# Kernel optimization log

Hardware: AMD Instinct MI355X
Metric: run time of the kernel (lower is better)

Reference implementation:

```python
import jax, jax.numpy as jnp
import numpy as np

EPS = 1e-8  # torch CosineSimilarity default eps

B, T, D, K = 16, 1024, 2048, 64


def setup_inputs() -> dict:
    key = jax.random.key(0)
    k1, k2, k3 = jax.random.split(key, 3)
    inputs = jax.random.normal(k1, (B, T, D), dtype=jnp.float32)
    class_avgs = jax.random.normal(k2, (K, D), dtype=jnp.float32)
    labels = jax.random.randint(k3, (B, T), 0, K, dtype=jnp.int64)
    return {"inputs": inputs, "class_avgs": class_avgs, "labels": labels}


def _simrel_forward(inputs, class_avgs, labels):
    # inputs: [B, T, D]; class_avgs: [K, D]; labels: [B, T] int
    # Faithful training-mode forward: sequential running-mean prototype
    # update per token (row-major over batch then sequence), cosine sims
    # computed against the prototype state *before* each token's update.
    b, t, d = inputs.shape
    k = class_avgs.shape[0]
    vecs = inputs.reshape(b * t, d)
    labs = labels.reshape(b * t)
    class_ids = jnp.arange(k)

    def step(carry, xs):
        avgs, counts = carry          # [K, D], [K]
        vec, label = xs               # [D], scalar int
        nv = jnp.maximum(jnp.sqrt(jnp.sum(vec * vec)), EPS)
        na = jnp.maximum(jnp.sqrt(jnp.sum(avgs * avgs, axis=1)), EPS)  # [K]
        cos = (avgs @ vec) / (na * nv)                                 # [K]
        is_inf = jnp.any(jnp.isinf(avgs), axis=1)                      # [K]
        self_sim = jnp.sum(vec * vec) / (nv * nv)  # cosine(vec, vec)
        is_label = class_ids == label
        sims = jnp.where(is_inf, jnp.where(is_label, self_sim, -1.0), cos)
        # running-mean update of the labeled class prototype
        c = counts[label]
        old = avgs[label]
        new_row = jnp.where(is_inf[label], vec, (old * c + vec) / (c + 1.0))
        avgs = avgs.at[label].set(new_row)
        counts = counts.at[label].add(1.0)
        return (avgs, counts), sims

    counts0 = jnp.zeros((k,), dtype=inputs.dtype)
    (_, _), sims = jax.lax.scan(step, (class_avgs, counts0), (vecs, labs))
    return sims.reshape(b, t, k)


def reference(inputs, class_avgs, labels):
    return _simrel_forward(inputs, class_avgs, labels)
```

## Files before the change

### kernel.cpp

```cpp
#include <hip/hip_runtime.h>
#include <hip/hip_bf16.h>

#define N_TOK 16384
#define DIM 2048
#define KCLS 64
#define JRANGES 32
#define RANGE 512
#define KC 64
#define EPS 1e-8f

typedef short bf16x8 __attribute__((ext_vector_type(8)));
typedef unsigned short u16x8 __attribute__((ext_vector_type(8)));
typedef float f32x4 __attribute__((ext_vector_type(4)));

__device__ __forceinline__ unsigned short f2bf(float f) {
    unsigned u = __float_as_uint(f);
    u += 0x7fffu + ((u >> 16) & 1u);
    return (unsigned short)(u >> 16);
}
__device__ __forceinline__ float bf2f(unsigned short s) {
    return __uint_as_float(((unsigned)s) << 16);
}

__device__ __forceinline__ float dpp_sum64(float x) {
    x += __int_as_float(__builtin_amdgcn_update_dpp(0, __float_as_int(x), 0x111, 0xf, 0xf, true));
    x += __int_as_float(__builtin_amdgcn_update_dpp(0, __float_as_int(x), 0x112, 0xf, 0xf, true));
    x += __int_as_float(__builtin_amdgcn_update_dpp(0, __float_as_int(x), 0x114, 0xf, 0xf, true));
    x += __int_as_float(__builtin_amdgcn_update_dpp(0, __float_as_int(x), 0x118, 0xf, 0xf, true));
    x += __int_as_float(__builtin_amdgcn_update_dpp(0, __float_as_int(x), 0x142, 0xf, 0xf, true));
    x += __int_as_float(__builtin_amdgcn_update_dpp(0, __float_as_int(x), 0x143, 0xf, 0xf, true));
    return x;
}

__global__ __launch_bounds__(256) void prep_kernel(
    const float* __restrict__ x, unsigned short* __restrict__ xb,
    float* __restrict__ vnorm2, const int* __restrict__ raw,
    int* __restrict__ lab, float* __restrict__ n2snap) {
    int bid = blockIdx.x, tid = threadIdx.x;
    if (bid < 64) {
        __shared__ int not64;
        if (tid == 0) not64 = 0;
        __syncthreads();
        int n0 = bid * 256 + tid;
        int lo = raw[2 * n0], hi = raw[2 * n0 + 1];
        if (hi != 0 || lo < 0 || lo >= KCLS) atomicOr(&not64, 1);
        __syncthreads();
        lab[n0] = not64 ? raw[n0] : raw[2 * n0];
    } else if (bid < 72) {
        n2snap[(bid - 64) * 256 + tid] = 0.f;
    }
    int w4 = tid >> 6, lane = tid & 63;
    int n = bid * 4 + w4;
    const float* v = x + (size_t)n * DIM;
    unsigned short* o = xb + (size_t)n * DIM;
    float p = 0.f;
#pragma unroll
    for (int it = 0; it < 8; it++) {
        float4 a = *(const float4*)(v + it * 256 + lane * 4);
        p = fmaf(a.x, a.x, p); p = fmaf(a.y, a.y, p);
        p = fmaf(a.z, a.z, p); p = fmaf(a.w, a.w, p);
        ushort4 h = make_ushort4(f2bf(a.x), f2bf(a.y), f2bf(a.z), f2bf(a.w));
        *(ushort4*)(o + it * 256 + lane * 4) = h;
    }
    p = dpp_sum64(p);
    if (lane == 63) vnorm2[n] = p;
}

__global__ __launch_bounds__(256) void partials_kernel(
    const unsigned short* __restrict__ xb, const int* __restrict__ lab,
    float* __restrict__ spart, int* __restrict__ cnt_range) {
    __shared__ unsigned char ll[RANGE];
    __shared__ short ml[RANGE];
    __shared__ int wt[4];

    int bid = blockIdx.x;
    int j = bid & 31, k = bid >> 5;
    int t = threadIdx.x, lane = t & 63, w = t >> 6;

    int2 lp = *(const int2*)(lab + j * RANGE + 2 * t);
    ll[2 * t] = (unsigned char)lp.x;
    ll[2 * t + 1] = (unsigned char)lp.y;
    int m0 = (lp.x == k) ? 1 : 0;
    int m1 = (lp.y == k) ? 1 : 0;
    int cnt = m0 + m1;
    int pre = cnt;
    for (int s = 1; s < 64; s <<= 1) {
        int v = __shfl_up(pre, s, 64);
        if (lane >= s) pre += v;
    }
    if (lane == 63) wt[w] = pre;
    __syncthreads();
    int woff = 0, nm = 0;
#pragma unroll
    for (int i = 0; i < 4; i++) { if (i < w) woff += wt[i]; nm += wt[i]; }
    {
        int wr = woff + pre - cnt;
        if (m0) ml[wr++] = (short)(2 * t);
        if (m1) ml[wr] = (short)(2 * t + 1);
    }
    __syncthreads();
    if (t == 0) cnt_range[j * KCLS + k] = nm;

    float acc[8] = {0, 0, 0, 0, 0, 0, 0, 0};
    for (int m = 0; m < nm; m++) {
        const unsigned short* r = xb + (size_t)(j * RANGE + (int)ml[m]) * DIM + t * 8;
        u16x8 hv = *(const u16x8*)r;
#pragma unroll
        for (int i = 0; i < 8; i++) acc[i] += bf2f(hv[i]);
    }
    float* dst = spart + ((size_t)j * KCLS + k) * DIM + t * 8;
    *(float4*)dst = make_float4(acc[0], acc[1], acc[2], acc[3]);
    *(float4*)(dst + 4) = make_float4(acc[4], acc[5], acc[6], acc[7]);
}

__global__ __launch_bounds__(256) void scan_kernel(
    const float* __restrict__ avgs, float* __restrict__ spart,
    unsigned short* __restrict__ Sb, float* __restrict__ n2snap,
    const int* __restrict__ cnt_range, int* __restrict__ cnt_before) {
    int t = blockIdx.x * 256 + threadIdx.x;
    int lane = threadIdx.x & 63;
    int k = t >> 9;
    int d4 = t & 511;
    int d = d4 * 4;
    float4 run = {0, 0, 0, 0};
    int cb = 0;
    float4 init = *(const float4*)(avgs + (size_t)k * DIM + d);
    for (int j = 0; j < JRANGES; j++) {
        size_t idx = ((size_t)j * KCLS + k) * DIM + d;
        float4 part = *(const float4*)(spart + idx);
        float4 w = (cb == 0) ? init : run;
        *(ushort4*)(Sb + idx) = make_ushort4(f2bf(w.x), f2bf(w.y), f2bf(w.z), f2bf(w.w));
        float s = 0.f;
        s = fmaf(w.x, w.x, s); s = fmaf(w.y, w.y, s);
        s = fmaf(w.z, w.z, s); s = fmaf(w.w, w.w, s);
        s = dpp_sum64(s);
        if (lane == 63) atomicAdd(&n2snap[j * KCLS + k], s);
        if (d4 == 0) cnt_before[j * KCLS + k] = cb;
        run.x += part.x; run.y += part.y; run.z += part.z; run.w += part.w;
        cb += cnt_range[j * KCLS + k];
    }
}

__device__ __forceinline__ void stage_panel(
    const unsigned short* __restrict__ src, short* dst, int nunits,
    int t, int kcoff) {
#pragma unroll
    for (int i = 0; i < 2; i++) {
        int u = t + 512 * i;
        if (u < nunits) {
            int row = u >> 3, gsw = u & 7;
            int g = gsw ^ (row & 7);
            const unsigned short* s = src + (size_t)row * DIM + kcoff + g * 8;
            __builtin_amdgcn_global_load_lds(
                (__attribute__((address_space(1))) void*)s,
                (__attribute__((address_space(3))) void*)(dst + u * 8),
                16, 0, 0);
        }
    }
}

__global__ __launch_bounds__(512, 4) void gemm_kernel(
    const unsigned short* __restrict__ xb, const unsigned short* __restrict__ Sb,
    float* __restrict__ D0, unsigned short* __restrict__ Gbf) {
    __shared__ short PI[2][128 * KC];
    __shared__ short PJ[2][128 * KC];
    static const char TIa[14] = {0,1,1,2,2,2,3,3,3,3, 0,1,2,3};
    static const char TJa[14] = {0,0,1,0,1,2,0,1,2,3, 0,0,0,0};

    int bid = blockIdx.x;
    int xcd = bid & 7;
    int q = bid >> 3;
    int j = xcd + 8 * (q / 14);
    int tt = q % 14;
    int I = TIa[tt], J = TJa[tt];
    bool isD = (tt >= 10);
    bool diag = (!isD) && (I == J);
    int start = j * RANGE;
    int t = threadIdx.x, lane = t & 63, w = t >> 6;
    int rw = w & 3, cw = w >> 2;
    int NCF = isD ? 2 : 4;
    int colbase = isD ? cw * 32 : cw * 64;

    f32x4 acc[2][4];
#pragma unroll
    for (int a = 0; a < 2; a++)
#pragma unroll
        for (int b = 0; b < 4; b++) acc[a][b] = (f32x4){0.f, 0.f, 0.f, 0.f};

    const unsigned short* srcI = xb + (size_t)(start + I * 128) * DIM;
    const unsigned short* srcJ = isD ? (Sb + (size_t)(j * KCLS) * DIM)
                                     : (xb + (size_t)(start + J * 128) * DIM);
    int nJu = isD ? 512 : 1024;

    stage_panel(srcI, PI[0], 1024, t, 0);
    if (!diag) stage_panel(srcJ, PJ[0], nJu, t, 0);
    __syncthreads();

    for (int kc = 0; kc < DIM / KC; kc++) {
        int cur = kc & 1;
        if (kc + 1 < DIM / KC) {
            stage_panel(srcI, PI[cur ^ 1], 1024, t, (kc + 1) * KC);
            if (!diag) stage_panel(srcJ, PJ[cur ^ 1], nJu, t, (kc + 1) * KC);
        }
        const short* PA = PI[cur];
        const short* PB = diag ? PI[cur] : PJ[cur];
#pragma unroll
        for (int kk = 0; kk < 2; kk++) {
            int kb = kk * 32 + (lane >> 4) * 8;
            int ra = rw * 32 + (lane & 15);
            bf16x8 a0 = *(const bf16x8*)&PA[ra * KC + (kb ^ ((ra & 7) << 3))];
            int ra1 = ra + 16;
            bf16x8 a1 = *(const bf16x8*)&PA[ra1 * KC + (kb ^ ((ra1 & 7) << 3))];
#pragma unroll
            for (int f = 0; f < 4; f++) {
                if (f < NCF) {
                    int rb = colbase + f * 16 + (lane & 15);
                    bf16x8 bb = *(const bf16x8*)&PB[rb * KC + (kb ^ ((rb & 7) << 3))];
                    acc[0][f] = __builtin_amdgcn_mfma_f32_16x16x32_bf16(a0, bb, acc[0][f], 0, 0, 0);
                    acc[1][f] = __builtin_amdgcn_mfma_f32_16x16x32_bf16(a1, bb, acc[1][f], 0, 0, 0);
                }
            }
        }
        __syncthreads();
    }

    if (!isD) {
        size_t gbase = (size_t)j * (512 * 512);
        short* TT = &PI[0][0];
#pragma unroll
        for (int rf = 0; rf < 2; rf++)
#pragma unroll
            for (int f = 0; f < 4; f++)
#pragma unroll
                for (int r = 0; r < 4; r++) {
                    int lr = rw * 32 + rf * 16 + (lane >> 4) * 4 + r;
                    int lc = colbase + f * 16 + (lane & 15);
                    unsigned short hv = f2bf(acc[rf][f][r]);
                    Gbf[gbase + (size_t)(I * 128 + lr) * 512 + J * 128 + lc] = hv;
                    if (I != J)
                        TT[lc * 128 + (lr ^ ((lc & 15) << 3))] = (short)hv;
                }
        if (I != J) {
            __syncthreads();
#pragma unroll
            for (int i = 0; i < 4; i++) {
                int u = t + 512 * i;
                int tr = u >> 4, tc = u & 15;
                u16x8 v = *(const u16x8*)&TT[tr * 128 + ((tc * 8) ^ ((tr & 15) << 3))];
                *(u16x8*)&Gbf[gbase + (size_t)(J * 128 + tr) * 512 + I * 128 + tc * 8] = v;
            }
        }
    } else {
#pragma unroll
        for (int rf = 0; rf < 2; rf++)
#pragma unroll
            for (int f = 0; f < 2; f++)
#pragma unroll
                for (int r = 0; r < 4; r++) {
                    int grow = start + I * 128 + rw * 32 + rf * 16 + (lane >> 4) * 4 + r;
                    int gcol = colbase + f * 16 + (lane & 15);
                    D0[(size_t)grow * KCLS + gcol] = acc[rf][f][r];
                }
    }
}

__global__ __launch_bounds__(512) void finalize_kernel(
    const int* __restrict__ lab, const float* __restrict__ D0,
    const unsigned short* __restrict__ Gbf, const float* __restrict__ vnorm2,
    const float* __restrict__ n2snap, const int* __restrict__ cnt_before,
    float* __restrict__ out) {
    __shared__ unsigned char lbl[RANGE];
    __shared__ short evl[RANGE];
    __shared__ short evcnt_s[8];
    __shared__ short evoff_s[9];
    __shared__ float corrb[8][RANGE];
    __shared__ float cntb[8][RANGE];
    __shared__ float rdv[RANGE];
    __shared__ float invna[RANGE + 8];
    __shared__ unsigned char vgs[8];

    int bid = blockIdx.x;
    int g = bid >> 5, jr = bid & 31;
    int g8 = g * 8;
    int start = jr * RANGE;
    int t = threadIdx.x, lane = t & 63, w = t >> 6;
    int c = g8 + w;

    lbl[t] = (unsigned char)lab[start + t];
    if (t < 8) vgs[t] = (cnt_before[jr * KCLS + g8 + t] == 0) ? 1 : 0;
    __syncthreads();

    unsigned char myl[8];
    int cntL = 0;
#pragma unroll
    for (int i = 0; i < 8; i++) {
        myl[i] = lbl[lane * 8 + i];
        cntL += (myl[i] == c) ? 1 : 0;
    }
    int pre = cntL;
    for (int s = 1; s < 64; s <<= 1) {
        int v = __shfl_up(pre, s, 64);
        if (lane >= s) pre += v;
    }
    int tot = __shfl(pre, 63, 64);
    if (lane == 63) evcnt_s[w] = (short)tot;
    __syncthreads();
    if (t == 0) {
        int s = 0;
        for (int i = 0; i < 8; i++) { evoff_s[i] = (short)s; s += evcnt_s[i]; }
        evoff_s[8] = (short)s;
    }
    __syncthreads();
    int off = evoff_s[w], m = evcnt_s[w];
    {
        int wr = off + (pre - cntL);
#pragma unroll
        for (int i = 0; i < 8; i++)
            if (myl[i] == c) evl[wr++] = (short)(lane * 8 + i);
    }
    __syncthreads();

    const unsigned short* grb = Gbf + (size_t)jr * 262144;
    int vg = vgs[w];
#pragma unroll 1
    for (int chk = 0; chk < 8; chk++) {
        int tk = chk * 64 + lane;
        float corr = 0.f;
        int cnt = 0;
#pragma unroll 1
        for (int i = 0; i < m; i++) {
            int e = evl[off + i];
            float gv = bf2f(grb[(size_t)e * 512 + tk]);
            bool after = (tk > e);
            corr += after ? gv : 0.f;
            cnt += after ? 1 : 0;
        }
        corrb[w][tk] = corr;
        cntb[w][tk] = (float)cnt;
        if ((int)lbl[tk] == c) {
            float d0v = vg ? 0.f : D0[(size_t)(start + tk) * KCLS + c];
            rdv[off + cnt] = d0v + corr;
        }
    }
    __syncthreads();

    if (t < 8) {
        int o = evoff_s[t], mm = evcnt_s[t];
        int vgt = vgs[t];
        float n2 = n2snap[jr * KCLS + g8 + t];
        invna[o + t] = 1.0f / fmaxf(sqrtf(n2), EPS);
        for (int i = 1; i <= mm; i++) {
            int e = evl[o + i - 1];
            float xn2 = vnorm2[start + e];
            if (vgt && i == 1) n2 = xn2;
            else n2 += 2.f * rdv[o + i - 1] + xn2;
            invna[o + t + i] = 1.0f / fmaxf(sqrtf(n2), EPS);
        }
    }
    __syncthreads();

    {
        float4 d0a = *(const float4*)&D0[(size_t)(start + t) * KCLS + g8];
        float4 d0b = *(const float4*)&D0[(size_t)(start + t) * KCLS + g8 + 4];
        float d0[8] = {d0a.x, d0a.y, d0a.z, d0a.w, d0b.x, d0b.y, d0b.z, d0b.w};
        float nvinv = 1.0f / fmaxf(sqrtf(vnorm2[start + t]), EPS);
        float o8[8];
#pragma unroll
        for (int cc = 0; cc < 8; cc++) {
            float corr = corrb[cc][t];
            int cnt = (int)cntb[cc][t];
            float dot = (vgs[cc] && cnt > 0) ? corr : (d0[cc] + corr);
            o8[cc] = dot * invna[evoff_s[cc] + cc + cnt] * nvinv;
        }
        float4 oa = {o8[0], o8[1], o8[2], o8[3]};
        float4 ob = {o8[4], o8[5], o8[6], o8[7]};
        float* op = &out[(size_t)(start + t) * KCLS + g8];
        *(float4*)op = oa;
        *(float4*)(op + 4) = ob;
    }
}

extern "C" void kernel_launch(void* const* d_in, const int* in_sizes, int n_in,
                              void* d_out, int out_size, void* d_ws, size_t ws_size,
                              hipStream_t stream) {
    const float* inputs = (const float*)d_in[0];
    const float* class_avgs = (const float*)d_in[1];
    const int* labels_raw = (const int*)d_in[2];
    float* out = (float*)d_out;
    char* ws = (char*)d_ws;

    size_t off = 0;
    int* lab = (int*)(ws + off);          off += (size_t)N_TOK * 4;
    int* cnt_range = (int*)(ws + off);    off += (size_t)JRANGES * KCLS * 4;
    int* cnt_before = (int*)(ws + off);   off += (size_t)JRANGES * KCLS * 4;
    float* n2snap = (float*)(ws + off);   off += (size_t)JRANGES * KCLS * 4;
    float* vnorm2 = (float*)(ws + off);   off += (size_t)N_TOK * 4;
    off = (off + 255) & ~(size_t)255;
    unsigned short* Xb = (unsigned short*)(ws + off);
    off += (size_t)N_TOK * DIM * 2;
    unsigned short* Sb = (unsigned short*)(ws + off);
    off += (size_t)JRANGES * KCLS * DIM * 2;
    float* D0 = (float*)(ws + off);       off += (size_t)N_TOK * KCLS * 4;
    unsigned short* Gbf = (unsigned short*)(ws + off);
    off += (size_t)JRANGES * 512 * 512 * 2;
    float* spart = (float*)(ws + off);    off += (size_t)JRANGES * KCLS * DIM * 4;

    prep_kernel<<<N_TOK / 4, 256, 0, stream>>>(inputs, Xb, vnorm2, labels_raw,
                                               lab, n2snap);
    partials_kernel<<<JRANGES * KCLS, 256, 0, stream>>>(Xb, lab, spart, cnt_range);
    scan_kernel<<<(KCLS * (DIM / 4)) / 256, 256, 0, stream>>>(class_avgs, spart, Sb,
                                                              n2snap, cnt_range,
                                                              cnt_before);
    gemm_kernel<<<14 * JRANGES, 512, 0, stream>>>(Xb, Sb, D0, Gbf);
    finalize_kernel<<<8 * JRANGES, 512, 0, stream>>>(lab, D0, Gbf, vnorm2, n2snap,
                                                     cnt_before, out);
}
```

Baseline: 153.2 us.

## Split K across warp halves with 64x64 warp tiles in Gram GEMM

For the token-token Gram tiles, each of the 8 warps now computes a 64x64 quadrant over half of each 64-wide K chunk, instead of a 32x64 strip over the full chunk. The two K-halves are then summed through shared memory before the bf16 store and transpose. The goal is to cut LDS fragment loads per MFMA (4 A plus 4 B loads for 16 MFMAs). The cost is a larger accumulator register footprint (64 floats), which may strain the 4-blocks-per-CU launch bound, plus an extra reduction pass with two added barriers.

```diff
diff --git a/kernel.cpp b/kernel.cpp
--- a/kernel.cpp
+++ b/kernel.cpp
@@ -162,8 +162,7 @@
 __global__ __launch_bounds__(512, 4) void gemm_kernel(
     const unsigned short* __restrict__ xb, const unsigned short* __restrict__ Sb,
     float* __restrict__ D0, unsigned short* __restrict__ Gbf) {
-    __shared__ short PI[2][128 * KC];
-    __shared__ short PJ[2][128 * KC];
+    __shared__ short SMEM[4][128 * KC];
     static const char TIa[14] = {0,1,1,2,2,2,3,3,3,3, 0,1,2,3};
     static const char TJa[14] = {0,0,1,0,1,2,0,1,2,3, 0,0,0,0};
 
@@ -177,13 +176,10 @@
     bool diag = (!isD) && (I == J);
     int start = j * RANGE;
     int t = threadIdx.x, lane = t & 63, w = t >> 6;
-    int rw = w & 3, cw = w >> 2;
-    int NCF = isD ? 2 : 4;
-    int colbase = isD ? cw * 32 : cw * 64;
-
-    f32x4 acc[2][4];
-#pragma unroll
-    for (int a = 0; a < 2; a++)
+
+    f32x4 acc[4][4];
+#pragma unroll
+    for (int a = 0; a < 4; a++)
 #pragma unroll
         for (int b = 0; b < 4; b++) acc[a][b] = (f32x4){0.f, 0.f, 0.f, 0.f};
 
@@ -192,29 +188,51 @@
                                      : (xb + (size_t)(start + J * 128) * DIM);
     int nJu = isD ? 512 : 1024;
 
-    stage_panel(srcI, PI[0], 1024, t, 0);
-    if (!diag) stage_panel(srcJ, PJ[0], nJu, t, 0);
-    __syncthreads();
+    stage_panel(srcI, SMEM[0], 1024, t, 0);
+    if (!diag) stage_panel(srcJ, SMEM[2], nJu, t, 0);
+    __syncthreads();
+
+    int qr = w & 1, qc = (w >> 1) & 1, ks = w >> 2;
+    int rw = w & 3, cw = w >> 2;
 
     for (int kc = 0; kc < DIM / KC; kc++) {
         int cur = kc & 1;
         if (kc + 1 < DIM / KC) {
-            stage_panel(srcI, PI[cur ^ 1], 1024, t, (kc + 1) * KC);
-            if (!diag) stage_panel(srcJ, PJ[cur ^ 1], nJu, t, (kc + 1) * KC);
-        }
-        const short* PA = PI[cur];
-        const short* PB = diag ? PI[cur] : PJ[cur];
-#pragma unroll
-        for (int kk = 0; kk < 2; kk++) {
-            int kb = kk * 32 + (lane >> 4) * 8;
-            int ra = rw * 32 + (lane & 15);
-            bf16x8 a0 = *(const bf16x8*)&PA[ra * KC + (kb ^ ((ra & 7) << 3))];
-            int ra1 = ra + 16;
-            bf16x8 a1 = *(const bf16x8*)&PA[ra1 * KC + (kb ^ ((ra1 & 7) << 3))];
-#pragma unroll
-            for (int f = 0; f < 4; f++) {
-                if (f < NCF) {
-                    int rb = colbase + f * 16 + (lane & 15);
+            stage_panel(srcI, SMEM[cur ^ 1], 1024, t, (kc + 1) * KC);
+            if (!diag) stage_panel(srcJ, SMEM[2 + (cur ^ 1)], nJu, t, (kc + 1) * KC);
+        }
+        const short* PA = SMEM[cur];
+        const short* PB = diag ? SMEM[cur] : SMEM[2 + cur];
+        if (!isD) {
+            int kb = ks * 32 + (lane >> 4) * 8;
+            bf16x8 Af[4], Bf[4];
+#pragma unroll
+            for (int af = 0; af < 4; af++) {
+                int ra = qr * 64 + af * 16 + (lane & 15);
+                Af[af] = *(const bf16x8*)&PA[ra * KC + (kb ^ ((ra & 7) << 3))];
+            }
+#pragma unroll
+            for (int bf = 0; bf < 4; bf++) {
+                int rb = qc * 64 + bf * 16 + (lane & 15);
+                Bf[bf] = *(const bf16x8*)&PB[rb * KC + (kb ^ ((rb & 7) << 3))];
+            }
+#pragma unroll
+            for (int af = 0; af < 4; af++)
+#pragma unroll
+                for (int bf = 0; bf < 4; bf++)
+                    acc[af][bf] = __builtin_amdgcn_mfma_f32_16x16x32_bf16(
+                        Af[af], Bf[bf], acc[af][bf], 0, 0, 0);
+        } else {
+#pragma unroll
+            for (int kk = 0; kk < 2; kk++) {
+                int kb = kk * 32 + (lane >> 4) * 8;
+                int ra = rw * 32 + (lane & 15);
+                bf16x8 a0 = *(const bf16x8*)&PA[ra * KC + (kb ^ ((ra & 7) << 3))];
+                int ra1 = ra + 16;
+                bf16x8 a1 = *(const bf16x8*)&PA[ra1 * KC + (kb ^ ((ra1 & 7) << 3))];
+#pragma unroll
+                for (int f = 0; f < 2; f++) {
+                    int rb = cw * 32 + f * 16 + (lane & 15);
                     bf16x8 bb = *(const bf16x8*)&PB[rb * KC + (kb ^ ((rb & 7) << 3))];
                     acc[0][f] = __builtin_amdgcn_mfma_f32_16x16x32_bf16(a0, bb, acc[0][f], 0, 0, 0);
                     acc[1][f] = __builtin_amdgcn_mfma_f32_16x16x32_bf16(a1, bb, acc[1][f], 0, 0, 0);
@@ -225,21 +243,44 @@
     }
 
     if (!isD) {
+        float* red = (float*)SMEM;
+        if (ks == 1) {
+#pragma unroll
+            for (int af = 0; af < 4; af++)
+#pragma unroll
+                for (int bf = 0; bf < 4; bf++)
+                    *(f32x4*)&red[(w - 4) * 4096 + (af * 4 + bf) * 256 + lane * 4] =
+                        acc[af][bf];
+        }
+        __syncthreads();
+        if (ks == 0) {
+#pragma unroll
+            for (int af = 0; af < 4; af++)
+#pragma unroll
+                for (int bf = 0; bf < 4; bf++) {
+                    f32x4 v = *(const f32x4*)&red[w * 4096 + (af * 4 + bf) * 256 + lane * 4];
+                    acc[af][bf] += v;
+                }
+        }
+        __syncthreads();
+
         size_t gbase = (size_t)j * (512 * 512);
-        short* TT = &PI[0][0];
-#pragma unroll
-        for (int rf = 0; rf < 2; rf++)
-#pragma unroll
-            for (int f = 0; f < 4; f++)
-#pragma unroll
-                for (int r = 0; r < 4; r++) {
-                    int lr = rw * 32 + rf * 16 + (lane >> 4) * 4 + r;
-                    int lc = colbase + f * 16 + (lane & 15);
-                    unsigned short hv = f2bf(acc[rf][f][r]);
-                    Gbf[gbase + (size_t)(I * 128 + lr) * 512 + J * 128 + lc] = hv;
-                    if (I != J)
-                        TT[lc * 128 + (lr ^ ((lc & 15) << 3))] = (short)hv;
-                }
+        short* TT = &SMEM[0][0];
+        if (ks == 0) {
+#pragma unroll
+            for (int af = 0; af < 4; af++)
+#pragma unroll
+                for (int bf = 0; bf < 4; bf++)
+#pragma unroll
+                    for (int r = 0; r < 4; r++) {
+                        int lr = qr * 64 + af * 16 + (lane >> 4) * 4 + r;
+                        int lc = qc * 64 + bf * 16 + (lane & 15);
+                        unsigned short hv = f2bf(acc[af][bf][r]);
+                        Gbf[gbase + (size_t)(I * 128 + lr) * 512 + J * 128 + lc] = hv;
+                        if (I != J)
+                            TT[lc * 128 + (lr ^ ((lc & 15) << 3))] = (short)hv;
+                    }
+        }
         if (I != J) {
             __syncthreads();
 #pragma unroll
@@ -258,7 +299,7 @@
 #pragma unroll
                 for (int r = 0; r < 4; r++) {
                     int grow = start + I * 128 + rw * 32 + rf * 16 + (lane >> 4) * 4 + r;
-                    int gcol = colbase + f * 16 + (lane & 15);
+                    int gcol = cw * 32 + f * 16 + (lane & 15);
                     D0[(size_t)grow * KCLS + gcol] = acc[rf][f][r];
                 }
     }
```

After: 154.2 us. About the same (+0.6%).
